# Kernel tuning notes

Hardware: AMD Instinct MI355X
Metric: run time of the kernel (lower is better)

The kernel has to match this reference:

```python
import jax, jax.numpy as jnp
import numpy as np

NEIGHBORHOOD_SIZE = 3
EPS_NORM = 1e-8   # torch CosineSimilarity eps
EPS_DEN = 1e-6


def setup_inputs() -> dict:
    key = jax.random.key(0)
    k1, k2 = jax.random.split(key)
    B, T, C = 8, 2048, 128
    x = jax.random.normal(k1, (B, T, C), dtype=jnp.float32)
    mapping = jnp.sort(jax.random.randint(k2, (B, T), 0, 64), axis=-1).astype(jnp.int64)
    return {"x": x, "mapping": mapping}


def reference(x, mapping):
    B, T, C = x.shape
    # Normalize once, then a single GEMM gives all pairwise cosine sims
    # (avoids the naive B x T x T x C broadcast).
    norms = jnp.linalg.norm(x, axis=-1, keepdims=True)          # [B,T,1]
    xn = x / jnp.maximum(norms, EPS_NORM)
    cos_pred = jnp.einsum('btc,bsc->bts', xn, xn)               # [B,T,T]

    m1 = mapping[:, :, None]                                    # [B,T,1]
    m2 = mapping[:, None, :]                                    # [B,1,T]
    cos_target = (m1 == m2).astype(cos_pred.dtype)              # [B,T,T]

    triu = jnp.triu(jnp.ones((T, T), dtype=bool), k=1)[None]    # strict upper triangle
    neighbor = jnp.abs(m1 - m2) <= NEIGHBORHOOD_SIZE
    padding = (m1 != 0) & (m2 != 0)
    mask = triu & neighbor & padding                             # [B,T,T]

    pred = jnp.where(mask, cos_pred, 0.0)
    tgt = jnp.where(mask, cos_target, 0.0)
    sq = (pred - tgt) ** 2
    loss = sq.sum() / (mask.astype(cos_pred.dtype).sum() + EPS_DEN)
    return loss
```

## Files before the change

### kernel.cpp

```cpp
#include <hip/hip_runtime.h>


#define TT 2048
#define CC 128
#define TM 64
#define SLOTS 4
#define NTILES 256
#define TOTAL_BLK (NTILES * SLOTS)
#define NORM_BLKS 4096
#define TBL_BLKS 64

typedef unsigned short ushort_t;
typedef __attribute__((ext_vector_type(8))) short v8s;
typedef __attribute__((ext_vector_type(4))) float v4f;

__device__ __forceinline__ ushort_t f2bf(float f) {
    unsigned u = __float_as_uint(f);
    return (ushort_t)((u + 0x7FFFu + ((u >> 16) & 1u)) >> 16);
}

__global__ void __launch_bounds__(256) k_prep(const float* __restrict__ x,
                                              const int* __restrict__ map,
                                              ushort_t* __restrict__ xnb,
                                              int* __restrict__ last_tbl) {
    const int bid = blockIdx.x;
    const int tid = threadIdx.x;

    if (bid < NORM_BLKS) {
        const int wave = tid >> 6, lane = tid & 63;
        const int row  = bid * 4 + wave;
        float2 v = ((const float2*)(x + (size_t)row * CC))[lane];
        float ss = v.x * v.x + v.y * v.y;
        #pragma unroll
        for (int off = 32; off; off >>= 1) ss += __shfl_xor(ss, off);
        const float rn = 1.0f / fmaxf(sqrtf(ss), 1e-8f);
        const unsigned lo = f2bf(v.x * rn), hi = f2bf(v.y * rn);
        ((unsigned*)(xnb + (size_t)row * CC))[lane] = lo | (hi << 16);
    } else {
        const int row = (bid - NORM_BLKS) * 256 + tid;
        const int b   = row >> 11, t = row & (TT - 1);
        const int* mb = map + b * TT;
        const int m   = mb[t];
        const int mn  = (t == TT - 1) ? 64 : mb[t + 1];
        for (int v = m; v < mn; ++v) last_tbl[b * 64 + v] = t;
    }
}

__global__ void __launch_bounds__(256) k_tile(const ushort_t* __restrict__ xnb,
                                              const int* __restrict__ map,
                                              const int* __restrict__ last_tbl,
                                              float* __restrict__ psum,
                                              int* __restrict__ pcnt) {
    __shared__ __align__(16) ushort_t As[TM * CC];
    __shared__ __align__(16) ushort_t Bs[TM * CC];
    __shared__ int mt_s[TM], et_s[TM], ms_s[TM];
    __shared__ float wsum[4];

    const int tile = blockIdx.x;
    const int slot = blockIdx.y;
    const int tid  = threadIdx.x;
    const int lane = tid & 63;
    const int wave = tid >> 6;
    const int b    = tile >> 5;
    const int t0   = (tile & 31) * TM;
    const int* mb  = map + b * TT;
    const ushort_t* xb = xnb + (size_t)(b * TT) * CC;

    int s_base = t0 + slot * TM;

    #pragma unroll
    for (int i = 0; i < 4; ++i) {
        const int pbase = wave * 256 + i * 64;
        const int p = pbase + lane;
        const int row = p >> 4;
        const int sl  = (p & 15) ^ (row & 7);
        __builtin_amdgcn_global_load_lds(
            (const __attribute__((address_space(1))) void*)(xb + (size_t)(t0 + row) * CC + sl * 8),
            (__attribute__((address_space(3))) void*)(&As[pbase * 8]), 16, 0, 0);
        const int srow = min(s_base + row, TT - 1);
        __builtin_amdgcn_global_load_lds(
            (const __attribute__((address_space(1))) void*)(xb + (size_t)srow * CC + sl * 8),
            (__attribute__((address_space(3))) void*)(&Bs[pbase * 8]), 16, 0, 0);
    }

    if (tid < TM) {
        const int t = t0 + tid;
        const int m = mb[t];
        int e = t;
        if (m != 0) e = last_tbl[b * 64 + min(m + 3, 63)];
        mt_s[tid] = m; et_s[tid] = e;
        ms_s[tid] = mb[min(s_base + tid, TT - 1)];
    }
    __syncthreads();

    int e = et_s[lane];
    #pragma unroll
    for (int off = 32; off; off >>= 1) e = max(e, __shfl_xor(e, off));
    const int emax = e;

    if (slot == 0 && wave == 0) {
        int c = et_s[lane] - (t0 + lane);
        #pragma unroll
        for (int off = 32; off; off >>= 1) c += __shfl_xor(c, off);
        if (lane == 0) pcnt[tile] = c;
    }

    if (s_base > emax) {
        if (tid == 0) psum[tile * SLOTS + slot] = 0.0f;
        return;
    }

    const int wr = wave >> 1, wc = wave & 1;
    const int r16 = lane & 15, kgrp = lane >> 4;
    const int rowA0 = wr * 32 + r16, rowA1 = rowA0 + 16;
    const int rowB0 = wc * 32 + r16, rowB1 = rowB0 + 16;

    float lsum = 0.0f;
    bool first = true;

    for (; s_base <= emax; s_base += SLOTS * TM) {
        if (!first) {
            __syncthreads();
            #pragma unroll
            for (int i = 0; i < 4; ++i) {
                const int pbase = wave * 256 + i * 64;
                const int p = pbase + lane;
                const int row = p >> 4;
                const int sl  = (p & 15) ^ (row & 7);
                __builtin_amdgcn_global_load_lds(
                    (const __attribute__((address_space(1))) void*)(xb + (size_t)(s_base + row) * CC + sl * 8),
                    (__attribute__((address_space(3))) void*)(&Bs[pbase * 8]), 16, 0, 0);
            }
            if (tid < TM) ms_s[tid] = mb[s_base + tid];
            __syncthreads();
        }
        first = false;

        v4f acc00 = {0,0,0,0}, acc01 = {0,0,0,0}, acc10 = {0,0,0,0}, acc11 = {0,0,0,0};
        #pragma unroll
        for (int kk = 0; kk < 4; ++kk) {
            const int sl = kk * 4 + kgrp;
            v8s a0 = *(const v8s*)&As[(rowA0 * 16 + (sl ^ (rowA0 & 7))) * 8];
            v8s a1 = *(const v8s*)&As[(rowA1 * 16 + (sl ^ (rowA1 & 7))) * 8];
            v8s b0 = *(const v8s*)&Bs[(rowB0 * 16 + (sl ^ (rowB0 & 7))) * 8];
            v8s b1 = *(const v8s*)&Bs[(rowB1 * 16 + (sl ^ (rowB1 & 7))) * 8];
            acc00 = __builtin_amdgcn_mfma_f32_16x16x32_bf16(a0, b0, acc00, 0, 0, 0);
            acc01 = __builtin_amdgcn_mfma_f32_16x16x32_bf16(a0, b1, acc01, 0, 0, 0);
            acc10 = __builtin_amdgcn_mfma_f32_16x16x32_bf16(a1, b0, acc10, 0, 0, 0);
            acc11 = __builtin_amdgcn_mfma_f32_16x16x32_bf16(a1, b1, acc11, 0, 0, 0);
        }

        #pragma unroll
        for (int fi = 0; fi < 2; ++fi) {
            #pragma unroll
            for (int fj = 0; fj < 2; ++fj) {
                const v4f a = fi == 0 ? (fj == 0 ? acc00 : acc01) : (fj == 0 ? acc10 : acc11);
                const int s_loc = wc * 32 + fj * 16 + r16;
                const int s     = s_base + s_loc;
                const int m_s   = ms_s[s_loc];
                #pragma unroll
                for (int r = 0; r < 4; ++r) {
                    const int t_loc = wr * 32 + fi * 16 + kgrp * 4 + r;
                    const int t     = t0 + t_loc;
                    const int m_t   = mt_s[t_loc];
                    if ((m_t != 0) & (s > t) & (s <= et_s[t_loc])) {
                        const float d = a[r] - (m_s == m_t ? 1.0f : 0.0f);
                        lsum += d * d;
                    }
                }
            }
        }
    }

    #pragma unroll
    for (int off = 32; off; off >>= 1) lsum += __shfl_xor(lsum, off);
    if (lane == 0) wsum[wave] = lsum;
    __syncthreads();
    if (tid == 0) psum[tile * SLOTS + slot] = wsum[0] + wsum[1] + wsum[2] + wsum[3];
}

__global__ void __launch_bounds__(256) k_final(const float* __restrict__ psum,
                                               const int* __restrict__ pcnt,
                                               float* __restrict__ out,
                                               int n_sum, int n_cnt) {
    __shared__ double ssum[256];
    __shared__ long long scnt[256];
    double s = 0.0; long long c = 0;
    for (int i = threadIdx.x; i < n_sum; i += 256) s += (double)psum[i];
    for (int i = threadIdx.x; i < n_cnt; i += 256) c += (long long)pcnt[i];
    ssum[threadIdx.x] = s; scnt[threadIdx.x] = c;
    __syncthreads();
    #pragma unroll
    for (int off = 128; off; off >>= 1) {
        if (threadIdx.x < off) {
            ssum[threadIdx.x] += ssum[threadIdx.x + off];
            scnt[threadIdx.x] += scnt[threadIdx.x + off];
        }
        __syncthreads();
    }
    if (threadIdx.x == 0) out[0] = (float)(ssum[0] / ((double)scnt[0] + 1e-6));
}

extern "C" void kernel_launch(void* const* d_in, const int* in_sizes, int n_in,
                              void* d_out, int out_size, void* d_ws, size_t ws_size,
                              hipStream_t stream) {
    (void)n_in; (void)out_size; (void)ws_size;
    const float* x   = (const float*)d_in[0];
    const int*   map = (const int*)d_in[1];
    float* out = (float*)d_out;

    const int n_rows = in_sizes[1];

    ushort_t* xnb = (ushort_t*)d_ws;
    char*     p   = (char*)d_ws + (size_t)n_rows * CC * 2;
    int*      tbl = (int*)p;                    p += 8 * 64 * 4;
    float*    ps  = (float*)p;                  p += (size_t)TOTAL_BLK * 4;
    int*      pc  = (int*)p;

    k_prep <<<NORM_BLKS + TBL_BLKS, 256, 0, stream>>>(x, map, xnb, tbl);
    k_tile <<<dim3(NTILES, SLOTS), 256, 0, stream>>>(xnb, map, tbl, ps, pc);
    k_final<<<1, 256, 0, stream>>>(ps, pc, out, TOTAL_BLK, NTILES);
}
```

Measured before the change: 20.55 us.

## Store only row norms in prep; normalize and convert to bf16 inside tile kernel

```diff
diff --git a/kernel.cpp b/kernel.cpp
--- a/kernel.cpp
+++ b/kernel.cpp
@@ -14,14 +14,16 @@
 typedef __attribute__((ext_vector_type(8))) short v8s;
 typedef __attribute__((ext_vector_type(4))) float v4f;
 
-__device__ __forceinline__ ushort_t f2bf(float f) {
-    unsigned u = __float_as_uint(f);
-    return (ushort_t)((u + 0x7FFFu + ((u >> 16) & 1u)) >> 16);
+__device__ __forceinline__ unsigned pack2bf(float a, float b) {
+    unsigned ua = __float_as_uint(a), ub = __float_as_uint(b);
+    ua = (ua + 0x7FFFu + ((ua >> 16) & 1u)) >> 16;
+    ub = (ub + 0x7FFFu + ((ub >> 16) & 1u)) & 0xFFFF0000u;
+    return ua | ub;
 }
 
 __global__ void __launch_bounds__(256) k_prep(const float* __restrict__ x,
                                               const int* __restrict__ map,
-                                              ushort_t* __restrict__ xnb,
+                                              float* __restrict__ rn,
                                               int* __restrict__ last_tbl) {
     const int bid = blockIdx.x;
     const int tid = threadIdx.x;
@@ -33,9 +35,7 @@
         float ss = v.x * v.x + v.y * v.y;
         #pragma unroll
         for (int off = 32; off; off >>= 1) ss += __shfl_xor(ss, off);
-        const float rn = 1.0f / fmaxf(sqrtf(ss), 1e-8f);
-        const unsigned lo = f2bf(v.x * rn), hi = f2bf(v.y * rn);
-        ((unsigned*)(xnb + (size_t)row * CC))[lane] = lo | (hi << 16);
+        if (lane == 0) rn[row] = 1.0f / fmaxf(sqrtf(ss), 1e-8f);
     } else {
         const int row = (bid - NORM_BLKS) * 256 + tid;
         const int b   = row >> 11, t = row & (TT - 1);
@@ -46,7 +46,8 @@
     }
 }
 
-__global__ void __launch_bounds__(256) k_tile(const ushort_t* __restrict__ xnb,
+__global__ void __launch_bounds__(256) k_tile(const float* __restrict__ x,
+                                              const float* __restrict__ rn,
                                               const int* __restrict__ map,
                                               const int* __restrict__ last_tbl,
                                               float* __restrict__ psum,
@@ -64,24 +65,8 @@
     const int b    = tile >> 5;
     const int t0   = (tile & 31) * TM;
     const int* mb  = map + b * TT;
-    const ushort_t* xb = xnb + (size_t)(b * TT) * CC;
-
-    int s_base = t0 + slot * TM;
-
-    #pragma unroll
-    for (int i = 0; i < 4; ++i) {
-        const int pbase = wave * 256 + i * 64;
-        const int p = pbase + lane;
-        const int row = p >> 4;
-        const int sl  = (p & 15) ^ (row & 7);
-        __builtin_amdgcn_global_load_lds(
-            (const __attribute__((address_space(1))) void*)(xb + (size_t)(t0 + row) * CC + sl * 8),
-            (__attribute__((address_space(3))) void*)(&As[pbase * 8]), 16, 0, 0);
-        const int srow = min(s_base + row, TT - 1);
-        __builtin_amdgcn_global_load_lds(
-            (const __attribute__((address_space(1))) void*)(xb + (size_t)srow * CC + sl * 8),
-            (__attribute__((address_space(3))) void*)(&Bs[pbase * 8]), 16, 0, 0);
-    }
+    const float* xg = x + (size_t)(b * TT) * CC;
+    const float* rb = rn + b * TT;
 
     if (tid < TM) {
         const int t = t0 + tid;
@@ -89,7 +74,6 @@
         int e = t;
         if (m != 0) e = last_tbl[b * 64 + min(m + 3, 63)];
         mt_s[tid] = m; et_s[tid] = e;
-        ms_s[tid] = mb[min(s_base + tid, TT - 1)];
     }
     __syncthreads();
 
@@ -105,9 +89,22 @@
         if (lane == 0) pcnt[tile] = c;
     }
 
+    int s_base = t0 + slot * TM;
     if (s_base > emax) {
         if (tid == 0) psum[tile * SLOTS + slot] = 0.0f;
         return;
+    }
+
+    #pragma unroll
+    for (int q = 0; q < 8; ++q) {
+        const int f = tid + q * 256;
+        const int row = f >> 5, c4 = f & 31;
+        float4 v = ((const float4*)(xg + (size_t)(t0 + row) * CC))[c4];
+        const float r = rb[t0 + row];
+        const unsigned lo = pack2bf(v.x * r, v.y * r);
+        const unsigned hi = pack2bf(v.z * r, v.w * r);
+        uint2* dst = (uint2*)&As[((row * 16 + ((c4 >> 1) ^ (row & 7))) * 8) + (c4 & 1) * 4];
+        *dst = make_uint2(lo, hi);
     }
 
     const int wr = wave >> 1, wc = wave & 1;
@@ -116,25 +113,31 @@
     const int rowB0 = wc * 32 + r16, rowB1 = rowB0 + 16;
 
     float lsum = 0.0f;
-    bool first = true;
 
     for (; s_base <= emax; s_base += SLOTS * TM) {
-        if (!first) {
-            __syncthreads();
-            #pragma unroll
-            for (int i = 0; i < 4; ++i) {
-                const int pbase = wave * 256 + i * 64;
-                const int p = pbase + lane;
-                const int row = p >> 4;
-                const int sl  = (p & 15) ^ (row & 7);
-                __builtin_amdgcn_global_load_lds(
-                    (const __attribute__((address_space(1))) void*)(xb + (size_t)(s_base + row) * CC + sl * 8),
-                    (__attribute__((address_space(3))) void*)(&Bs[pbase * 8]), 16, 0, 0);
-            }
-            if (tid < TM) ms_s[tid] = mb[s_base + tid];
-            __syncthreads();
-        }
-        first = false;
+        float4 bv[8]; float brn[8];
+        #pragma unroll
+        for (int q = 0; q < 8; ++q) {
+            const int f = tid + q * 256;
+            const int row = f >> 5, c4 = f & 31;
+            bv[q]  = ((const float4*)(xg + (size_t)(s_base + row) * CC))[c4];
+            brn[q] = rb[s_base + row];
+        }
+        int msv = 0;
+        if (tid < TM) msv = mb[s_base + tid];
+        __syncthreads();
+
+        #pragma unroll
+        for (int q = 0; q < 8; ++q) {
+            const int f = tid + q * 256;
+            const int row = f >> 5, c4 = f & 31;
+            const unsigned lo = pack2bf(bv[q].x * brn[q], bv[q].y * brn[q]);
+            const unsigned hi = pack2bf(bv[q].z * brn[q], bv[q].w * brn[q]);
+            uint2* dst = (uint2*)&Bs[((row * 16 + ((c4 >> 1) ^ (row & 7))) * 8) + (c4 & 1) * 4];
+            *dst = make_uint2(lo, hi);
+        }
+        if (tid < TM) ms_s[tid] = msv;
+        __syncthreads();
 
         v4f acc00 = {0,0,0,0}, acc01 = {0,0,0,0}, acc10 = {0,0,0,0}, acc11 = {0,0,0,0};
         #pragma unroll
@@ -211,13 +214,13 @@
 
     const int n_rows = in_sizes[1];
 
-    ushort_t* xnb = (ushort_t*)d_ws;
-    char*     p   = (char*)d_ws + (size_t)n_rows * CC * 2;
-    int*      tbl = (int*)p;                    p += 8 * 64 * 4;
-    float*    ps  = (float*)p;                  p += (size_t)TOTAL_BLK * 4;
-    int*      pc  = (int*)p;
-
-    k_prep <<<NORM_BLKS + TBL_BLKS, 256, 0, stream>>>(x, map, xnb, tbl);
-    k_tile <<<dim3(NTILES, SLOTS), 256, 0, stream>>>(xnb, map, tbl, ps, pc);
+    char*  p   = (char*)d_ws;
+    float* rnw = (float*)p;                     p += (size_t)n_rows * 4;
+    int*   tbl = (int*)p;                       p += 8 * 64 * 4;
+    float* ps  = (float*)p;                     p += (size_t)TOTAL_BLK * 4;
+    int*   pc  = (int*)p;
+
+    k_prep <<<NORM_BLKS + TBL_BLKS, 256, 0, stream>>>(x, map, rnw, tbl);
+    k_tile <<<dim3(NTILES, SLOTS), 256, 0, stream>>>(x, rnw, map, tbl, ps, pc);
     k_final<<<1, 256, 0, stream>>>(ps, pc, out, TOTAL_BLK, NTILES);
 }
```

Measured after the change: 20.48 us. Within noise of the previous version (-0.3%).
